# Performance work log

Measured on AMD Instinct MI355X. Metric: run time of the kernel, lower is better.

Reference implementation:

```python
import jax, jax.numpy as jnp
import numpy as np

LATENT_DIM = 256
BOOK_SIZE = 8192


def setup_inputs() -> dict:
    key = jax.random.key(0)
    k1, k2 = jax.random.split(key)
    z_e = jax.random.normal(k1, (16, LATENT_DIM, 32, 32), dtype=jnp.float32)
    codebook = jax.random.normal(k2, (BOOK_SIZE, LATENT_DIM), dtype=jnp.float32)
    return {"z_e": z_e, "codebook": codebook}


def reference(z_e, codebook):
    # NCHW -> NHWC -> (B*H*W, D)
    flat_z = jnp.transpose(z_e, (0, 2, 3, 1)).reshape(-1, LATENT_DIM)
    # squared euclidean distance via matmul: ||z||^2 + ||e||^2 - 2 z.e
    dist = (
        jnp.sum(flat_z ** 2, axis=1, keepdims=True)
        + jnp.sum(codebook ** 2, axis=1)
        - 2.0 * flat_z @ codebook.T
    )  # (N, book_size)
    indices = jnp.argmin(dist, axis=1)          # (N,)
    z_q = codebook[indices]                      # (N, D) gather
    return z_q, indices
```

## Files before the change

kernel.cpp:

```cpp
#include <hip/hip_runtime.h>
#include <stdint.h>

#define NROWS 16384
#define NCODES 8192
#define DIM 256
#define EPS_S 0.4f
#define SM 0.8f

typedef __attribute__((ext_vector_type(8))) short bf16x8;
typedef __attribute__((ext_vector_type(16))) float f32x16;
typedef unsigned int uint32;

__device__ __forceinline__ unsigned short f2bf(float f) {
  union { float f; unsigned int u; } v; v.f = f;
  unsigned int u = v.u;
  return (unsigned short)((u + 0x7FFFu + ((u >> 16) & 1u)) >> 16);
}

__device__ __forceinline__ unsigned long long packdi(float d, int idx) {
  unsigned int u = __float_as_uint(d);
  u = (u & 0x80000000u) ? ~u : (u | 0x80000000u);
  return ((unsigned long long)u << 32) | (unsigned int)idx;
}
__device__ __forceinline__ unsigned long long u64min(unsigned long long a,
                                                     unsigned long long b) {
  return a < b ? a : b;
}
__device__ __forceinline__ unsigned long long shflx64(unsigned long long v, int m) {
  int lo = __shfl_xor((int)(unsigned int)v, m);
  int hi = __shfl_xor((int)(v >> 32), m);
  return ((unsigned long long)(unsigned int)hi << 32) | (unsigned int)lo;
}
__device__ __forceinline__ uint32 umax(uint32 a, uint32 b) { return a > b ? a : b; }
__device__ __forceinline__ uint32 umin(uint32 a, uint32 b) { return a < b ? a : b; }

__device__ __forceinline__ void glds16(const ushort* g, ushort* l) {
  __builtin_amdgcn_global_load_lds(
      (const __attribute__((address_space(1))) unsigned int*)g,
      (__attribute__((address_space(3))) unsigned int*)l, 16, 0, 0);
}

__global__ __launch_bounds__(256) void prep(const float* __restrict__ z,
                                            const float* __restrict__ cb,
                                            float* __restrict__ flatz,
                                            ushort* __restrict__ zb,
                                            ushort* __restrict__ eb,
                                            float* __restrict__ enorm) {
  __shared__ float t[32][33];
  const int blk = blockIdx.x;
  if (blk < 4096) {
    const int tx = threadIdx.x & 31, ty = threadIdx.x >> 5;
    const int ht = blk & 31, ct = (blk >> 5) & 7, b = blk >> 8;
    const float* src = z + (size_t)b * 262144 + (size_t)(ct * 32) * 1024 + ht * 32;
#pragma unroll
    for (int i = 0; i < 4; ++i) {
      int c = ty + i * 8;
      t[c][tx] = src[c * 1024 + tx];
    }
    __syncthreads();
#pragma unroll
    for (int i = 0; i < 4; ++i) {
      int hw = ty + i * 8;
      int row = b * 1024 + ht * 32 + hw;
      float v = t[tx][hw];
      flatz[(size_t)row * 256 + ct * 32 + tx] = v;
      zb[(size_t)row * 256 + ct * 32 + tx] = f2bf(v);
    }
  } else {
    const int lane = threadIdx.x & 63, wave = threadIdx.x >> 6;
    const int code = (blk - 4096) * 4 + wave;
    float4 v = *(const float4*)(cb + (size_t)code * 256 + lane * 4);
    ushort4 o;
    o.x = f2bf(v.x); o.y = f2bf(v.y); o.z = f2bf(v.z); o.w = f2bf(v.w);
    *(ushort4*)(eb + (size_t)code * 256 + lane * 4) = o;
    float ss = v.x * v.x + v.y * v.y + v.z * v.z + v.w * v.w;
#pragma unroll
    for (int s = 1; s < 64; s <<= 1) ss += __shfl_xor(ss, s);
    if (lane == 0) enorm[code] = ss;
  }
}

__device__ __forceinline__ void init_acc(f32x16 acc[4][2], const float* en,
                                         int ot, int wm, int lg) {
#pragma unroll
  for (int m = 0; m < 4; ++m) {
    const float* ep = en + ot * 256 + wm * 128 + m * 32 + 4 * lg;
    float4 e0 = *(const float4*)(ep);
    float4 e1 = *(const float4*)(ep + 8);
    float4 e2 = *(const float4*)(ep + 16);
    float4 e3 = *(const float4*)(ep + 24);
    f32x16 c0;
    c0[0]  = 1024.f - 0.5f * e0.x; c0[1]  = 1024.f - 0.5f * e0.y;
    c0[2]  = 1024.f - 0.5f * e0.z; c0[3]  = 1024.f - 0.5f * e0.w;
    c0[4]  = 1024.f - 0.5f * e1.x; c0[5]  = 1024.f - 0.5f * e1.y;
    c0[6]  = 1024.f - 0.5f * e1.z; c0[7]  = 1024.f - 0.5f * e1.w;
    c0[8]  = 1024.f - 0.5f * e2.x; c0[9]  = 1024.f - 0.5f * e2.y;
    c0[10] = 1024.f - 0.5f * e2.z; c0[11] = 1024.f - 0.5f * e2.w;
    c0[12] = 1024.f - 0.5f * e3.x; c0[13] = 1024.f - 0.5f * e3.y;
    c0[14] = 1024.f - 0.5f * e3.z; c0[15] = 1024.f - 0.5f * e3.w;
    acc[m][0] = c0; acc[m][1] = c0;
  }
}

__device__ __forceinline__ void epilogue(const f32x16 acc[4][2],
                                         uint32* __restrict__ bm, int cg,
                                         int ot, int zrow0, int wm, int wn,
                                         int l31, int lg) {
  const int cid0 = cg * 128 + ot * 16 + wm * 8;
#pragma unroll
  for (int n = 0; n < 2; ++n) {
    uint32 res[8];
#pragma unroll
    for (int m = 0; m < 4; ++m)
#pragma unroll
      for (int hc = 0; hc < 2; ++hc) {
        uint32 m1 = 0, m2 = 0;
#pragma unroll
        for (int p = 0; p < 8; ++p) {
          uint32 id = (uint32)((p & 3) | (lg << 2) | ((p >> 2) << 3));
          uint32 pv = (__float_as_uint(acc[m][n][hc * 8 + p]) & ~31u) | id;
          m2 = umax(m2, umin(m1, pv));
          m1 = umax(m1, pv);
        }
        uint32 o1 = (uint32)__shfl_xor((int)m1, 32);
        uint32 o2 = (uint32)__shfl_xor((int)m2, 32);
        m2 = umax(umax(m2, o2), umin(m1, o1));
        m1 = umax(m1, o1);
        float s1 = __uint_as_float(m1 & ~31u);
        float s2 = __uint_as_float(m2 & ~31u);
        res[m * 2 + hc] = (s1 - s2 > SM) ? (m1 | 16u) : m1;
      }
    const int zr = zrow0 + wn * 64 + n * 32 + l31;
    uint4 o;
    o.x = lg ? res[4] : res[0];
    o.y = lg ? res[5] : res[1];
    o.z = lg ? res[6] : res[2];
    o.w = lg ? res[7] : res[3];
    *(uint4*)(bm + (size_t)zr * 512 + cid0 + lg * 4) = o;
  }
}

__global__ __launch_bounds__(512, 2) void vq_gemm(const ushort* __restrict__ eb,
                                                  const ushort* __restrict__ zb,
                                                  const float* __restrict__ enorm,
                                                  uint32* __restrict__ bm) {
  __shared__ __align__(16) ushort As[4 * 8192];
  __shared__ __align__(16) ushort Bs[4 * 8192];
  __shared__ __align__(16) float en[2048];
  const int tid = threadIdx.x;
  const int wave = tid >> 6, lane = tid & 63;
  const int wm = wave >> 2, wn = wave & 3;
  const int l31 = lane & 31, lg = lane >> 5;
  const int y = blockIdx.x & 63, cg = blockIdx.x >> 6;
  const int code00 = cg * 2048;
  const int zrow0 = y * 256;

  *(float4*)&en[tid * 4] = *(const float4*)(enorm + code00 + tid * 4);
  __syncthreads();

  const int u0 = tid, u1 = tid + 512;
  const ushort* aU0 = eb + (size_t)(code00 + (u0 >> 2)) * 256 +
                      ((u0 & 3) ^ ((u0 >> 2) & 3)) * 8;
  const ushort* aU1 = eb + (size_t)(code00 + (u1 >> 2)) * 256 +
                      ((u1 & 3) ^ ((u1 >> 2) & 3)) * 8;
  const ushort* bU0 = zb + (size_t)(zrow0 + (u0 >> 2)) * 256 +
                      ((u0 & 3) ^ ((u0 >> 2) & 3)) * 8;
  const ushort* bU1 = zb + (size_t)(zrow0 + (u1 >> 2)) * 256 +
                      ((u1 & 3) ^ ((u1 >> 2) & 3)) * 8;
  ushort* aL = As + wave * 512;
  ushort* bL = Bs + wave * 512;

  glds16(aU0, aL);
  glds16(aU1, aL + 4096);
  glds16(bU0, bL);
  glds16(bU1, bL + 4096);
  glds16(aU0 + 32, aL + 8192);
  glds16(aU1 + 32, aL + 8192 + 4096);
  glds16(bU0 + 32, bL + 8192);
  glds16(bU1 + 32, bL + 8192 + 4096);

  f32x16 acc[4][2];
  init_acc(acc, en, 0, wm, lg);

  asm volatile("s_waitcnt vmcnt(4)" ::: "memory");
  __builtin_amdgcn_s_barrier();
  asm volatile("" ::: "memory");

  const int sw = lane & 3;
  const int colu0 = ((0 | lg) ^ sw) * 8;
  const int colu1 = ((2 | lg) ^ sw) * 8;
  const int arow_u = (wm * 128 + l31) * 32;
  const int brow_u = (wn * 64 + l31) * 32;

#pragma unroll 1
  for (int ot = 0; ot < 8; ++ot) {
    const size_t aoff = (size_t)ot * 65536;
    if (ot > 0) {
      epilogue(acc, bm, cg, ot - 1, zrow0, wm, wn, l31, lg);
      init_acc(acc, en, ot, wm, lg);
    }
#pragma unroll
    for (int cc = 0; cc < 8; ++cc) {
      const int slot = cc & 3;
      if (cc < 6) {
        const int s2 = (cc + 2) & 3;
        const int ko = (cc + 2) * 32;
        glds16(aU0 + aoff + ko, aL + s2 * 8192);
        glds16(aU1 + aoff + ko, aL + s2 * 8192 + 4096);
        glds16(bU0 + ko, bL + s2 * 8192);
        glds16(bU1 + ko, bL + s2 * 8192 + 4096);
      } else if (ot < 7) {
        const int s2 = (cc + 2) & 3;
        const int ko = (cc - 6) * 32;
        glds16(aU0 + aoff + 65536 + ko, aL + s2 * 8192);
        glds16(aU1 + aoff + 65536 + ko, aL + s2 * 8192 + 4096);
        glds16(bU0 + ko, bL + s2 * 8192);
        glds16(bU1 + ko, bL + s2 * 8192 + 4096);
      }
      bf16x8 a0[4], a1[4], b0[2], b1[2];
#pragma unroll
      for (int m = 0; m < 4; ++m) {
        a0[m] = *(const bf16x8*)&As[slot * 8192 + arow_u + m * 1024 + colu0];
        a1[m] = *(const bf16x8*)&As[slot * 8192 + arow_u + m * 1024 + colu1];
      }
#pragma unroll
      for (int n = 0; n < 2; ++n) {
        b0[n] = *(const bf16x8*)&Bs[slot * 8192 + brow_u + n * 1024 + colu0];
        b1[n] = *(const bf16x8*)&Bs[slot * 8192 + brow_u + n * 1024 + colu1];
      }
      __builtin_amdgcn_s_setprio(1);
#pragma unroll
      for (int m = 0; m < 4; ++m)
#pragma unroll
        for (int n = 0; n < 2; ++n)
          acc[m][n] = __builtin_amdgcn_mfma_f32_32x32x16_bf16(a0[m], b0[n],
                                                              acc[m][n], 0, 0, 0);
#pragma unroll
      for (int m = 0; m < 4; ++m)
#pragma unroll
        for (int n = 0; n < 2; ++n)
          acc[m][n] = __builtin_amdgcn_mfma_f32_32x32x16_bf16(a1[m], b1[n],
                                                              acc[m][n], 0, 0, 0);
      __builtin_amdgcn_s_setprio(0);
      if (cc < 6) {
        asm volatile("s_waitcnt vmcnt(4)" ::: "memory");
      } else if (ot < 7) {
        asm volatile("s_waitcnt vmcnt(4)" ::: "memory");
      } else {
        asm volatile("s_waitcnt vmcnt(0)" ::: "memory");
      }
      __builtin_amdgcn_s_barrier();
      asm volatile("" ::: "memory");
    }
  }
  epilogue(acc, bm, cg, 7, zrow0, wm, wn, l31, lg);
}

__device__ __forceinline__ unsigned long long chunk_exact(
    int chunk, const float* __restrict__ zrow, const float* __restrict__ cb,
    const float* __restrict__ enorm, int lane) {
  const int code = chunk * 16 + (lane >> 2);
  const float* zp = zrow + (lane & 3) * 64;
  const float* cp = cb + (size_t)code * 256 + (lane & 3) * 64;
  float s = 0.f;
#pragma unroll
  for (int d = 0; d < 64; d += 4) {
    float4 zv = *(const float4*)(zp + d);
    float4 cv = *(const float4*)(cp + d);
    s = fmaf(zv.x, cv.x, s); s = fmaf(zv.y, cv.y, s);
    s = fmaf(zv.z, cv.z, s); s = fmaf(zv.w, cv.w, s);
  }
  s += __shfl_xor(s, 1);
  s += __shfl_xor(s, 2);
  float dist = fmaf(-2.f, s, enorm[code]);
  unsigned long long key = ((lane & 3) == 0) ? packdi(dist, code) : ~0ull;
#pragma unroll
  for (int m = 1; m < 64; m <<= 1) key = u64min(key, shflx64(key, m));
  return key;
}

__global__ __launch_bounds__(256) void vq_sel(const uint32* __restrict__ bm,
                                              const float* __restrict__ flatz,
                                              const float* __restrict__ cb,
                                              const float* __restrict__ enorm,
                                              float* __restrict__ zq,
                                              float* __restrict__ oidx) {
  const int lane = threadIdx.x & 63;
  const int row = blockIdx.x * 4 + (threadIdx.x >> 6);
  uint4 va = *(const uint4*)(bm + (size_t)row * 512 + lane * 8);
  uint4 vb = *(const uint4*)(bm + (size_t)row * 512 + lane * 8 + 4);
  uint32 v[8] = {va.x, va.y, va.z, va.w, vb.x, vb.y, vb.z, vb.w};
  uint32 m1 = 0, m2 = 0; int ch = 0;
#pragma unroll
  for (int s = 0; s < 8; ++s) {
    uint32 pv = v[s];
    m2 = umax(m2, umin(m1, pv));
    ch = (pv > m1) ? (lane * 8 + s) : ch;
    m1 = umax(m1, pv);
  }
#pragma unroll
  for (int m = 1; m < 64; m <<= 1) {
    uint32 o1 = (uint32)__shfl_xor((int)m1, m);
    uint32 o2 = (uint32)__shfl_xor((int)m2, m);
    int oc = __shfl_xor(ch, m);
    m2 = umax(umax(m2, o2), umin(m1, o1));
    ch = (o1 > m1) ? oc : ch;
    m1 = umax(m1, o1);
  }
  float s1 = __uint_as_float(m1 & ~31u);
  float s2 = __uint_as_float(m2 & ~31u);
  int idx;
  if ((m1 & 16u) && (s1 - s2 > SM)) {
    idx = ch * 16 + (int)(m1 & 15u);
  } else {
    const float* zrow = flatz + (size_t)row * 256;
    unsigned long long key = chunk_exact(ch, zrow, cb, enorm, lane);
    float dbest;
    { unsigned int u = (unsigned int)(key >> 32);
      u = (u & 0x80000000u) ? (u & 0x7FFFFFFFu) : ~u;
      dbest = __uint_as_float(u); }
    float thr = (1024.f - 0.5f * dbest) - EPS_S;
#pragma unroll
    for (int s = 0; s < 8; ++s) {
      bool cand = __uint_as_float(v[s] & ~31u) >= thr;
      unsigned long long mk = __ballot(cand);
      while (mk) {
        int L = __ffsll(mk) - 1;
        mk &= mk - 1;
        int c2 = L * 8 + s;
        if (c2 == ch) continue;
        key = u64min(key, chunk_exact(c2, zrow, cb, enorm, lane));
      }
    }
    idx = (int)(key & 0xFFFFFFFFull);
  }
  if (lane == 0) oidx[row] = (float)idx;
  float4 val = *(const float4*)(cb + (size_t)idx * 256 + lane * 4);
  *(float4*)(zq + (size_t)row * 256 + lane * 4) = val;
}

extern "C" void kernel_launch(void* const* d_in, const int* in_sizes, int n_in,
                              void* d_out, int out_size, void* d_ws, size_t ws_size,
                              hipStream_t stream) {
  const float* z = (const float*)d_in[0];
  const float* cb = (const float*)d_in[1];
  char* ws = (char*)d_ws;
  ushort* zb = (ushort*)(ws);
  ushort* eb = (ushort*)(ws + (8u << 20));
  float* enorm = (float*)(ws + (12u << 20));
  uint32* bm = (uint32*)(ws + (13u << 20));
  float* zq = (float*)d_out;
  float* oidx = zq + (size_t)NROWS * DIM;
  float* flatz = zq;

  prep<<<4096 + NCODES / 4, 256, 0, stream>>>(z, cb, flatz, zb, eb, enorm);
  vq_gemm<<<256, 512, 0, stream>>>(eb, zb, enorm, bm);
  vq_sel<<<NROWS / 4, 256, 0, stream>>>(bm, flatz, cb, enorm, zq, oidx);
}
```

Measured before the change: 197.9 us.

## Deepen LDS prefetch to three stages and change LDS swizzle pattern

The global-to-LDS prefetch pipeline now runs three chunks ahead instead of two across the four LDS slots, and the wait counts are adjusted so that two chunks stay in flight. The XOR swizzle for the LDS layout now keys on a different row bit, (row>>1)&3, on both the store and read sides, aiming to cut LDS bank conflicts on the MFMA operand reads. The final barrier on the last iteration is dropped. With three chunks in flight and a barrier each step, the slot being overwritten is the one read in the previous step, so this relies on barrier ordering being correct.

```diff
diff --git a/kernel.cpp b/kernel.cpp
--- a/kernel.cpp
+++ b/kernel.cpp
@@ -160,41 +160,39 @@
 
   const int u0 = tid, u1 = tid + 512;
   const ushort* aU0 = eb + (size_t)(code00 + (u0 >> 2)) * 256 +
-                      ((u0 & 3) ^ ((u0 >> 2) & 3)) * 8;
+                      ((u0 & 3) ^ ((u0 >> 3) & 3)) * 8;
   const ushort* aU1 = eb + (size_t)(code00 + (u1 >> 2)) * 256 +
-                      ((u1 & 3) ^ ((u1 >> 2) & 3)) * 8;
+                      ((u1 & 3) ^ ((u1 >> 3) & 3)) * 8;
   const ushort* bU0 = zb + (size_t)(zrow0 + (u0 >> 2)) * 256 +
-                      ((u0 & 3) ^ ((u0 >> 2) & 3)) * 8;
+                      ((u0 & 3) ^ ((u0 >> 3) & 3)) * 8;
   const ushort* bU1 = zb + (size_t)(zrow0 + (u1 >> 2)) * 256 +
-                      ((u1 & 3) ^ ((u1 >> 2) & 3)) * 8;
+                      ((u1 & 3) ^ ((u1 >> 3) & 3)) * 8;
   ushort* aL = As + wave * 512;
   ushort* bL = Bs + wave * 512;
 
-  glds16(aU0, aL);
-  glds16(aU1, aL + 4096);
-  glds16(bU0, bL);
-  glds16(bU1, bL + 4096);
-  glds16(aU0 + 32, aL + 8192);
-  glds16(aU1 + 32, aL + 8192 + 4096);
-  glds16(bU0 + 32, bL + 8192);
-  glds16(bU1 + 32, bL + 8192 + 4096);
+#pragma unroll
+  for (int c = 0; c < 3; ++c) {
+    glds16(aU0 + c * 32, aL + c * 8192);
+    glds16(aU1 + c * 32, aL + c * 8192 + 4096);
+    glds16(bU0 + c * 32, bL + c * 8192);
+    glds16(bU1 + c * 32, bL + c * 8192 + 4096);
+  }
 
   f32x16 acc[4][2];
   init_acc(acc, en, 0, wm, lg);
 
-  asm volatile("s_waitcnt vmcnt(4)" ::: "memory");
+  asm volatile("s_waitcnt vmcnt(8)" ::: "memory");
   __builtin_amdgcn_s_barrier();
   asm volatile("" ::: "memory");
 
-  const int sw = lane & 3;
-  const int colu0 = ((0 | lg) ^ sw) * 8;
-  const int colu1 = ((2 | lg) ^ sw) * 8;
+  const int swz = (l31 >> 1) & 3;
+  const int colu0 = ((0 | lg) ^ swz) * 8;
+  const int colu1 = ((2 | lg) ^ swz) * 8;
   const int arow_u = (wm * 128 + l31) * 32;
   const int brow_u = (wn * 64 + l31) * 32;
 
 #pragma unroll 1
   for (int ot = 0; ot < 8; ++ot) {
-    const size_t aoff = (size_t)ot * 65536;
     if (ot > 0) {
       epilogue(acc, bm, cg, ot - 1, zrow0, wm, wn, l31, lg);
       init_acc(acc, en, ot, wm, lg);
@@ -202,20 +200,15 @@
 #pragma unroll
     for (int cc = 0; cc < 8; ++cc) {
       const int slot = cc & 3;
-      if (cc < 6) {
-        const int s2 = (cc + 2) & 3;
-        const int ko = (cc + 2) * 32;
-        glds16(aU0 + aoff + ko, aL + s2 * 8192);
-        glds16(aU1 + aoff + ko, aL + s2 * 8192 + 4096);
-        glds16(bU0 + ko, bL + s2 * 8192);
-        glds16(bU1 + ko, bL + s2 * 8192 + 4096);
-      } else if (ot < 7) {
-        const int s2 = (cc + 2) & 3;
-        const int ko = (cc - 6) * 32;
-        glds16(aU0 + aoff + 65536 + ko, aL + s2 * 8192);
-        glds16(aU1 + aoff + 65536 + ko, aL + s2 * 8192 + 4096);
-        glds16(bU0 + ko, bL + s2 * 8192);
-        glds16(bU1 + ko, bL + s2 * 8192 + 4096);
+      if (ot < 7 || cc <= 4) {
+        const int s2 = (cc + 3) & 3;
+        const size_t off = (size_t)((cc + 3) >> 3) * 65536 +
+                           (size_t)ot * 65536 + ((cc + 3) & 7) * 32;
+        const size_t boff = ((cc + 3) & 7) * 32;
+        glds16(aU0 + off, aL + s2 * 8192);
+        glds16(aU1 + off, aL + s2 * 8192 + 4096);
+        glds16(bU0 + boff, bL + s2 * 8192);
+        glds16(bU1 + boff, bL + s2 * 8192 + 4096);
       }
       bf16x8 a0[4], a1[4], b0[2], b1[2];
 #pragma unroll
@@ -242,15 +235,19 @@
           acc[m][n] = __builtin_amdgcn_mfma_f32_32x32x16_bf16(a1[m], b1[n],
                                                               acc[m][n], 0, 0, 0);
       __builtin_amdgcn_s_setprio(0);
-      if (cc < 6) {
+      if (ot < 7 || cc <= 4) {
+        asm volatile("s_waitcnt vmcnt(8)" ::: "memory");
+        __builtin_amdgcn_s_barrier();
+        asm volatile("" ::: "memory");
+      } else if (cc == 5) {
         asm volatile("s_waitcnt vmcnt(4)" ::: "memory");
-      } else if (ot < 7) {
-        asm volatile("s_waitcnt vmcnt(4)" ::: "memory");
-      } else {
+        __builtin_amdgcn_s_barrier();
+        asm volatile("" ::: "memory");
+      } else if (cc == 6) {
         asm volatile("s_waitcnt vmcnt(0)" ::: "memory");
-      }
-      __builtin_amdgcn_s_barrier();
-      asm volatile("" ::: "memory");
+        __builtin_amdgcn_s_barrier();
+        asm volatile("" ::: "memory");
+      }
     }
   }
   epilogue(acc, bm, cg, 7, zrow0, wm, wn, l31, lg);
```

New measurement: 182.7 us. -7.7%, faster.
